# Kernel optimization log

Measured on AMD Instinct MI355X. Metric: run time of the kernel, lower is better.

## Reference

```python
import jax, jax.numpy as jnp
import numpy as np
import math

NUM_CLASSES = 80
FPN_CH = 256
STEM = [256, 256, 256, 256]
C_IN = {"c3": 64, "c4": 160, "c5": 400}


def _conv(x, w, b, pad):
    # x: (B, Cin, H, W), w: (Cout, Cin, kh, kw)
    y = jax.lax.conv_general_dilated(
        x, w, window_strides=(1, 1), padding=[(pad, pad), (pad, pad)],
        dimension_numbers=("NCHW", "OIHW", "NCHW"))
    return y + b[None, :, None, None]


def _upsample2x(x):
    # F.interpolate(scale_factor=2), default mode='nearest'
    return jnp.repeat(jnp.repeat(x, 2, axis=2), 2, axis=3)


def _flatten_hw(x):
    # (B, C, H, W) -> (B, H*W, C)
    B, C, H, W = x.shape
    return x.reshape(B, C, H * W).transpose(0, 2, 1)


def setup_inputs() -> dict:
    key = jax.random.key(0)
    ks = iter(jax.random.split(key, 64))
    d = {}
    d["c3"] = jax.random.normal(next(ks), (2, 64, 64, 64), jnp.float32)
    d["c4"] = jax.random.normal(next(ks), (2, 160, 32, 32), jnp.float32)
    d["c5"] = jax.random.normal(next(ks), (2, 400, 16, 16), jnp.float32)

    def w(shape, std):
        return jax.random.normal(next(ks), shape, jnp.float32) * std

    # FPN lateral 1x1 convs and output 3x3 convs (default torch init ~ small)
    for lvl, cin in C_IN.items():
        n = lvl[1]
        d[f"lat{n}_w"] = w((FPN_CH, cin, 1, 1), 1.0 / math.sqrt(cin))
        d[f"lat{n}_b"] = jnp.zeros((FPN_CH,), jnp.float32)
        d[f"out{n}_w"] = w((FPN_CH, FPN_CH, 3, 3), 1.0 / math.sqrt(9 * FPN_CH))
        d[f"out{n}_b"] = jnp.zeros((FPN_CH,), jnp.float32)

    # Stem convs: init N(0, 0.01), bias 0 (per module code). Stacked (L, Cout, Cin, 3, 3).
    L = len(STEM)
    d["stem_cls_w"] = w((L, FPN_CH, FPN_CH, 3, 3), 0.01)
    d["stem_cls_b"] = jnp.zeros((L, FPN_CH), jnp.float32)
    d["stem_box_w"] = w((L, FPN_CH, FPN_CH, 3, 3), 0.01)
    d["stem_box_b"] = jnp.zeros((L, FPN_CH), jnp.float32)

    d["cls_w"] = w((NUM_CLASSES, FPN_CH, 3, 3), 1.0 / math.sqrt(9 * FPN_CH))
    d["cls_b"] = jnp.full((NUM_CLASSES,), -math.log(99.0), jnp.float32)
    d["box_w"] = w((4, FPN_CH, 3, 3), 1.0 / math.sqrt(9 * FPN_CH))
    d["box_b"] = jnp.zeros((4,), jnp.float32)
    d["ctr_w"] = w((1, FPN_CH, 3, 3), 1.0 / math.sqrt(9 * FPN_CH))
    d["ctr_b"] = jnp.zeros((1,), jnp.float32)
    return d


def reference(c3, c4, c5,
              lat3_w, lat3_b, lat4_w, lat4_b, lat5_w, lat5_b,
              out3_w, out3_b, out4_w, out4_b, out5_w, out5_b,
              stem_cls_w, stem_cls_b, stem_box_w, stem_box_b,
              cls_w, cls_b, box_w, box_b, ctr_w, ctr_b):
    # ---- FPN ----
    l3 = _conv(c3, lat3_w, lat3_b, 0)
    l4 = _conv(c4, lat4_w, lat4_b, 0)
    l5 = _conv(c5, lat5_w, lat5_b, 0)
    p5 = _conv(l5, out5_w, out5_b, 1)
    l4 = l4 + _upsample2x(l5)
    p4 = _conv(l4, out4_w, out4_b, 1)
    l3 = l3 + _upsample2x(l4)
    p3 = _conv(l3, out3_w, out3_b, 1)

    # ---- Prediction heads ----
    def head(feat):
        hc, hb = feat, feat
        for i in range(stem_cls_w.shape[0]):
            hc = jax.nn.relu(_conv(hc, stem_cls_w[i], stem_cls_b[i], 1))
            hb = jax.nn.relu(_conv(hb, stem_box_w[i], stem_box_b[i], 1))
        cls = _flatten_hw(_conv(hc, cls_w, cls_b, 1))      # (B, HW, num_classes)
        box = _flatten_hw(_conv(hb, box_w, box_b, 1))      # (B, HW, 4)
        ctr = _flatten_hw(_conv(hb, ctr_w, ctr_b, 1))      # (B, HW, 1)
        return cls, box, ctr

    outs = [head(p) for p in (p3, p4, p5)]
    cls_all = jnp.concatenate([o[0] for o in outs], axis=1)
    box_all = jnp.concatenate([o[1] for o in outs], axis=1)
    ctr_all = jnp.concatenate([o[2] for o in outs], axis=1)
    # pack: (B, total_locations, num_classes + 4 + 1)
    return jnp.concatenate([cls_all, box_all, ctr_all], axis=-1)
```

## Files before the change

### kernel.cpp

```cpp
#include <hip/hip_runtime.h>

typedef unsigned short u16;
typedef __attribute__((ext_vector_type(8))) __bf16 bf16x8;
typedef __attribute__((ext_vector_type(16))) float f32x16;

__device__ __forceinline__ float bf2f(u16 u) {
  union { unsigned i; float f; } x; x.i = ((unsigned)u) << 16; return x.f;
}
__device__ __forceinline__ u16 f2bf(float f) {
  union { float f; unsigned i; } x; x.f = f;
  unsigned r = x.i + 0x7FFFu + ((x.i >> 16) & 1u);
  return (u16)(r >> 16);
}
__device__ __forceinline__ bf16x8 ld8(const u16* p) {
  union { int2 i2[2]; bf16x8 v; } u;
  u.i2[0] = *(const int2*)p;
  u.i2[1] = *(const int2*)(p + 4);
  return u.v;
}

struct WJob { const float* src; u16* dst; int Cin, Cout, taps, NC, Cpad, special; };
struct WArgs {
  WJob j[16];
  const float *box_w, *ctr_w;
  const float *cls_b, *box_b, *ctr_b;
  float *bcls, *bbc;
};

__global__ __launch_bounds__(256) void wtrans_kernel(WArgs a) {
  WJob jb = a.j[blockIdx.y];
  int count = jb.taps * jb.NC * jb.Cpad * 64;
  for (int e = blockIdx.x * 256 + threadIdx.x; e < count; e += gridDim.x * 256) {
    int cw = e & 63;
    int r = e >> 6;
    int n = r % jb.Cpad;
    int q = r / jb.Cpad;
    int t = q % jb.taps;
    int cc = q / jb.taps;
    int ci = cc * 64 + cw;
    int nl = (n & ~63) + 2 * (n & 31) + ((n >> 5) & 1);
    float v = 0.f;
    if (jb.special) {
      if (ci < jb.Cin) {
        if (nl < 4) v = a.box_w[((size_t)nl * jb.Cin + ci) * jb.taps + t];
        else if (nl == 4) v = a.ctr_w[(size_t)ci * jb.taps + t];
      }
    } else if (nl < jb.Cout && ci < jb.Cin) {
      v = jb.src[((size_t)nl * jb.Cin + ci) * jb.taps + t];
    }
    jb.dst[e] = f2bf(v);
  }
  if (blockIdx.y == 0 && blockIdx.x == 0) {
    int t = threadIdx.x;
    if (t < 128) a.bcls[t] = (t < 80) ? a.cls_b[t] : 0.f;
    else if (t < 192) {
      int n = t - 128;
      a.bbc[n] = (n < 4) ? a.box_b[n] : (n == 4 ? a.ctr_b[0] : 0.f);
    }
  }
}

__global__ __launch_bounds__(256) void transpose_kernel(const float* __restrict__ c3,
                                                        const float* __restrict__ c4,
                                                        const float* __restrict__ c5,
                                                        u16* __restrict__ c3t,
                                                        u16* __restrict__ c4t,
                                                        u16* __restrict__ c5t) {
  int gid = blockIdx.x * 256 + threadIdx.x;
  const float* in; u16* out; int C, HW;
  if (gid < 524288) { in = c3; out = c3t; C = 64; HW = 4096; }
  else if (gid < 851968) { gid -= 524288; in = c4; out = c4t; C = 160; HW = 1024; }
  else { gid -= 851968; if (gid >= 204800) return; in = c5; out = c5t; C = 400; HW = 256; }
  int CHW = C * HW;
  int b = gid / CHW;
  int rem = gid - b * CHW;
  int c = rem / HW;
  int pos = rem - c * HW;
  out[((size_t)b * HW + pos) * C + c] = f2bf(in[gid]);
}

__global__ __launch_bounds__(256) void upadd2_kernel(u16* __restrict__ l3, u16* __restrict__ l4n,
                                                     const u16* __restrict__ l4,
                                                     const u16* __restrict__ l5) {
  int gid = blockIdx.x * 256 + threadIdx.x;
  if (gid < 524288) {
    int c = gid & 255; int m = gid >> 8;
    int b = m >> 10, pos = m & 1023;
    int y = pos >> 5, x = pos & 31;
    int sp = (b << 8) + ((y >> 1) << 4) + (x >> 1);
    l4n[gid] = f2bf(bf2f(l4[gid]) + bf2f(l5[(size_t)sp * 256 + c]));
  } else {
    int g2 = gid - 524288;
    int c = g2 & 255; int m = g2 >> 8;
    int b = m >> 12, pos = m & 4095;
    int y = pos >> 6, x = pos & 63;
    int sp2 = (b << 10) + ((y >> 1) << 5) + (x >> 1);
    int sp4 = (b << 8) + ((y >> 2) << 4) + (x >> 2);
    l3[g2] = f2bf(bf2f(l3[g2]) + bf2f(l4[(size_t)sp2 * 256 + c]) + bf2f(l5[(size_t)sp4 * 256 + c]));
  }
}

struct ConvP {
  const u16* src[2][3];
  const u16* wT[2][3];
  const float* bias[2][3];
  void* dst[2][3];
  int H[3], W[3], lgW[3], lgHW[3], pre[3], NC[3], Crow[3], locoff[3];
  int Cpad[2], Nvalid[2], choff[2], ny[2];
  int relu, direct;
};

#define APAD 68

#define TAPX(RB) do {                                                          \
    if (kk + 1 < ktot) {                                                       \
      writeB((kk + 1) & 1, RB);                                                \
      if (kk + 3 < ktot) loadB(kk + 3, RB);                                    \
    }                                                                          \
    const u16* ar = As + hpbase * APAD + koffs;                                \
    const u16* br0 = Bs[kk & 1] + (lane & 31) * APAD + koffs;                  \
    const u16* br1 = br0 + 32 * APAD;                                          \
    _Pragma("unroll")                                                          \
    for (int ks = 0; ks < 4; ++ks) {                                           \
      bf16x8 af = ld8(ar + ks * 16);                                           \
      acc[0] = __builtin_amdgcn_mfma_f32_32x32x16_bf16(af, ld8(br0 + ks * 16), acc[0], 0, 0, 0); \
      acc[1] = __builtin_amdgcn_mfma_f32_32x32x16_bf16(af, ld8(br1 + ks * 16), acc[1], 0, 0, 0); \
    }                                                                          \
    __syncthreads();                                                           \
    ++kk; ++cc;                                                                \
    if (cc < NCv) {                                                            \
      writeA(rA);                                                              \
      if (cc + 1 < NCv) loadA(cc + 1, rA);                                     \
      __syncthreads();                                                         \
    }                                                                          \
  } while (0)

__global__ __launch_bounds__(256, 3) void conv1_kernel(ConvP p) {
  constexpr int HALO_W = 8;
  constexpr int NA = 16 * 8 * 8;
  constexpr int NSLOT = 4;
  __shared__ u16 As[128 * APAD];
  __shared__ u16 Bs[2][64 * APAD];
  const int tid = threadIdx.x;
  const int br = blockIdx.z;
  if (blockIdx.y >= p.ny[br]) return;
  const int bx = blockIdx.x;
  const int lv = (bx >= p.pre[1]) + (bx >= p.pre[2]);
  const u16* __restrict__ src = p.src[br][lv];
  const u16* __restrict__ wT = p.wT[br][lv];
  const float* bias = p.bias[br][lv];
  void* dstv = p.dst[br][lv];
  const int H = p.H[lv], W = p.W[lv];
  const int lgWv = p.lgW[lv], lgHWv = p.lgHW[lv];
  const int NCv = p.NC[lv], Crow = p.Crow[lv];
  const int Cpadv = p.Cpad[br];
  const int ktot = NCv;
  const int nt = blockIdx.y * 64;
  const int wave = tid >> 6, lane = tid & 63;

  const int pidx = bx - p.pre[lv];
  const int lgppb = lgHWv - 7;
  const int lgnpx = lgWv - 3;
  const int batch = pidx >> lgppb;
  const int pp = pidx & ((1 << lgppb) - 1);
  const int py0 = (pp >> lgnpx) << 4;
  const int px0 = (pp & ((1 << lgnpx) - 1)) << 3;
  const size_t srcb = (size_t)batch * (1 << lgHWv) * Crow;

  f32x16 acc[2];
#pragma unroll
  for (int i = 0; i < 16; ++i) { acc[0][i] = 0.f; acc[1][i] = 0.f; }

  const int ml = wave * 32 + (lane & 31);
  const int my = ml >> 3, mx = ml & 7;
  const int koffs = (lane >> 5) << 3;
  const int hpbase = my * HALO_W + mx;

  int4 rA[NSLOT];
  int4 rB0[2], rB1[2];

  auto loadA = [&](int cc2, int4* r) {
    int kb = cc2 << 6;
#pragma unroll
    for (int s = 0; s < NSLOT; ++s) {
      int idx = s * 256 + tid;
      int4 v = make_int4(0, 0, 0, 0);
      int pos = idx >> 3, part = idx & 7;
      int hy = pos >> 3, hx = pos & 7;
      int gy = py0 + hy, gx = px0 + hx;
      int ch = kb + (part << 3);
      if ((unsigned)gy < (unsigned)H && (unsigned)gx < (unsigned)W && ch < Crow)
        v = *(const int4*)(src + srcb + (size_t)((gy << lgWv) + gx) * Crow + ch);
      r[s] = v;
    }
  };
  auto writeA = [&](const int4* r) {
#pragma unroll
    for (int s = 0; s < NSLOT; ++s) {
      int idx = s * 256 + tid;
      int pos = idx >> 3, part = idx & 7;
      u16* d = As + pos * APAD + (part << 3);
      *(int2*)d = make_int2(r[s].x, r[s].y);
      *(int2*)(d + 4) = make_int2(r[s].z, r[s].w);
    }
  };
  auto loadB = [&](int j, int4* r) {
    const u16* wsrc = wT + (((size_t)j * Cpadv + nt) << 6);
    r[0] = *(const int4*)(wsrc + ((tid >> 3) << 6) + ((tid & 7) << 3));
    r[1] = *(const int4*)(wsrc + (((tid >> 3) + 32) << 6) + ((tid & 7) << 3));
  };
  auto writeB = [&](int bufi, const int4* r) {
    u16* bb = Bs[bufi];
    u16* d0 = bb + (tid >> 3) * APAD + ((tid & 7) << 3);
    u16* d1 = bb + ((tid >> 3) + 32) * APAD + ((tid & 7) << 3);
    *(int2*)d0 = make_int2(r[0].x, r[0].y);
    *(int2*)(d0 + 4) = make_int2(r[0].z, r[0].w);
    *(int2*)d1 = make_int2(r[1].x, r[1].y);
    *(int2*)(d1 + 4) = make_int2(r[1].z, r[1].w);
  };

  loadA(0, rA);
  loadB(0, rB0);
  if (ktot > 1) loadB(1, rB1);
  writeA(rA);
  writeB(0, rB0);
  if (ktot > 2) loadB(2, rB0);
  if (NCv > 1) loadA(1, rA);
  __syncthreads();

  int kk = 0, cc = 0;
  while (true) {
    TAPX(rB1);
    if (kk >= ktot) break;
    TAPX(rB0);
    if (kk >= ktot) break;
  }

  const int col = lane & 31;
  const int rbs = 4 * (lane >> 5);
  const float bv0 = bias[nt + 2 * col];
  const float bv1 = bias[nt + 2 * col + 1];
#pragma unroll
  for (int r = 0; r < 16; ++r) {
    int m2 = wave * 32 + rbs + (r & 3) + 8 * (r >> 2);
    int posi = ((py0 + (m2 >> 3)) << lgWv) + px0 + (m2 & 7);
    float v0 = acc[0][r] + bv0;
    float v1 = acc[1][r] + bv1;
    unsigned pk = (unsigned)f2bf(v0) | ((unsigned)f2bf(v1) << 16);
    *(unsigned*)((u16*)dstv + ((size_t)(batch << lgHWv) + posi) * 256 + nt + 2 * col) = pk;
  }
}

#define TAP9(T, S) do {                                                        \
    constexpr int hpo_ = ((T) / 3 - 1) * 10 + ((T) % 3 - 1);                   \
    const u16* ar = As + (hpbase + hpo_) * APAD + koffs;                       \
    const u16* br0 = Bs[S] + (lane & 31) * APAD + koffs;                       \
    const u16* br1 = br0 + 32 * APAD;                                          \
    _Pragma("unroll")                                                          \
    for (int ks = 0; ks < 4; ++ks) {                                           \
      bf16x8 af = ld8(ar + ks * 16);                                           \
      acc[0] = __builtin_amdgcn_mfma_f32_32x32x16_bf16(af, ld8(br0 + ks * 16), acc[0], 0, 0, 0); \
      acc[1] = __builtin_amdgcn_mfma_f32_32x32x16_bf16(af, ld8(br1 + ks * 16), acc[1], 0, 0, 0); \
    }                                                                          \
  } while (0)

__global__ __launch_bounds__(256, 3) void conv9_kernel(ConvP p) {
  constexpr int HALO_W = 10;
  constexpr int NA = 18 * 10 * 8;
  constexpr int NSLOT = 6;
  __shared__ u16 As[180 * APAD];
  __shared__ u16 Bs[3][64 * APAD];
  const int tid = threadIdx.x;
  const int br = blockIdx.z;
  if (blockIdx.y >= p.ny[br]) return;
  const int bx = blockIdx.x;
  const int lv = (bx >= p.pre[1]) + (bx >= p.pre[2]);
  const u16* __restrict__ src = p.src[br][lv];
  const u16* __restrict__ wT = p.wT[br][lv];
  const float* bias = p.bias[br][lv];
  void* dstv = p.dst[br][lv];
  const int H = p.H[lv], W = p.W[lv];
  const int lgWv = p.lgW[lv], lgHWv = p.lgHW[lv];
  const int Crow = p.Crow[lv];
  const int Cpadv = p.Cpad[br];
  const int nt = blockIdx.y * 64;
  const int wave = tid >> 6, lane = tid & 63;

  const int pidx = bx - p.pre[lv];
  const int lgppb = lgHWv - 7;
  const int lgnpx = lgWv - 3;
  const int batch = pidx >> lgppb;
  const int pp = pidx & ((1 << lgppb) - 1);
  const int py0 = (pp >> lgnpx) << 4;
  const int px0 = (pp & ((1 << lgnpx) - 1)) << 3;
  const size_t srcb = (size_t)batch * (1 << lgHWv) * Crow;

  f32x16 acc[2];
#pragma unroll
  for (int i = 0; i < 16; ++i) { acc[0][i] = 0.f; acc[1][i] = 0.f; }

  const int ml = wave * 32 + (lane & 31);
  const int my = ml >> 3, mx = ml & 7;
  const int koffs = (lane >> 5) << 3;
  const int hpbase = (my + 1) * HALO_W + (mx + 1);

  int4 rA[NSLOT];
  int4 rB[6];

  auto loadA = [&](int cc2, int4* r) {
    int kb = cc2 << 6;
#pragma unroll
    for (int s = 0; s < NSLOT; ++s) {
      int idx = s * 256 + tid;
      int4 v = make_int4(0, 0, 0, 0);
      if (idx < NA) {
        int pos = idx >> 3, part = idx & 7;
        int hy = pos / HALO_W, hx = pos - hy * HALO_W;
        int gy = py0 + hy - 1, gx = px0 + hx - 1;
        int ch = kb + (part << 3);
        if ((unsigned)gy < (unsigned)H && (unsigned)gx < (unsigned)W && ch < Crow)
          v = *(const int4*)(src + srcb + (size_t)((gy << lgWv) + gx) * Crow + ch);
      }
      r[s] = v;
    }
  };
  auto writeA = [&](const int4* r) {
#pragma unroll
    for (int s = 0; s < NSLOT; ++s) {
      int idx = s * 256 + tid;
      if (idx < NA) {
        int pos = idx >> 3, part = idx & 7;
        u16* d = As + pos * APAD + (part << 3);
        *(int2*)d = make_int2(r[s].x, r[s].y);
        *(int2*)(d + 4) = make_int2(r[s].z, r[s].w);
      }
    }
  };
  auto loadB3 = [&](int j, int4* r) {
#pragma unroll
    for (int s = 0; s < 3; ++s) {
      const u16* wsrc = wT + (((size_t)(j + s) * Cpadv + nt) << 6);
      r[2 * s] = *(const int4*)(wsrc + ((tid >> 3) << 6) + ((tid & 7) << 3));
      r[2 * s + 1] = *(const int4*)(wsrc + (((tid >> 3) + 32) << 6) + ((tid & 7) << 3));
    }
  };
  auto writeB3 = [&](const int4* r) {
#pragma unroll
    for (int s = 0; s < 3; ++s) {
      u16* bb = Bs[s];
      u16* d0 = bb + (tid >> 3) * APAD + ((tid & 7) << 3);
      u16* d1 = bb + ((tid >> 3) + 32) * APAD + ((tid & 7) << 3);
      *(int2*)d0 = make_int2(r[2 * s].x, r[2 * s].y);
      *(int2*)(d0 + 4) = make_int2(r[2 * s].z, r[2 * s].w);
      *(int2*)d1 = make_int2(r[2 * s + 1].x, r[2 * s + 1].y);
      *(int2*)(d1 + 4) = make_int2(r[2 * s + 1].z, r[2 * s + 1].w);
    }
  };

  loadA(0, rA);
  loadB3(0, rB);
  writeA(rA);
  writeB3(rB);
  loadB3(3, rB);
  loadA(1, rA);
  __syncthreads();

  for (int cc = 0; cc < 4; ++cc) {
    TAP9(0, 0); TAP9(1, 1); TAP9(2, 2);
    __syncthreads();
    writeB3(rB);
    __syncthreads();
    loadB3(cc * 9 + 6, rB);
    TAP9(3, 0); TAP9(4, 1); TAP9(5, 2);
    __syncthreads();
    writeB3(rB);
    __syncthreads();
    if (cc * 9 + 9 < 36) loadB3(cc * 9 + 9, rB);
    TAP9(6, 0); TAP9(7, 1); TAP9(8, 2);
    __syncthreads();
    if (cc < 3) {
      writeB3(rB);
      writeA(rA);
      __syncthreads();
      loadB3(cc * 9 + 12, rB);
      if (cc < 2) loadA(cc + 2, rA);
    }
  }

  const int col = lane & 31;
  const int rbs = 4 * (lane >> 5);
  const int nbase = nt + 2 * col;
  const float bv0 = bias[nbase];
  const float bv1 = bias[nbase + 1];
#pragma unroll
  for (int r = 0; r < 16; ++r) {
    int m2 = wave * 32 + rbs + (r & 3) + 8 * (r >> 2);
    int posi = ((py0 + (m2 >> 3)) << lgWv) + px0 + (m2 & 7);
    float v0 = acc[0][r] + bv0;
    float v1 = acc[1][r] + bv1;
    if (p.relu) { v0 = fmaxf(v0, 0.f); v1 = fmaxf(v1, 0.f); }
    if (!p.direct) {
      unsigned pk = (unsigned)f2bf(v0) | ((unsigned)f2bf(v1) << 16);
      *(unsigned*)((u16*)dstv + ((size_t)(batch << lgHWv) + posi) * 256 + nbase) = pk;
    } else {
      float* dd = (float*)dstv + ((size_t)(batch * 5376 + p.locoff[lv] + posi)) * 85 + p.choff[br];
      if (nbase < p.Nvalid[br]) dd[nbase] = v0;
      if (nbase + 1 < p.Nvalid[br]) dd[nbase + 1] = v1;
    }
  }
}

extern "C" void kernel_launch(void* const* d_in, const int* in_sizes, int n_in,
                              void* d_out, int out_size, void* d_ws, size_t ws_size,
                              hipStream_t stream) {
  (void)in_sizes; (void)n_in; (void)out_size; (void)ws_size;
  const float* c3 = (const float*)d_in[0];
  const float* c4 = (const float*)d_in[1];
  const float* c5 = (const float*)d_in[2];
  const float* lat_w[3] = {(const float*)d_in[3], (const float*)d_in[7], (const float*)d_in[11]};
  const float* lat_b[3] = {(const float*)d_in[4], (const float*)d_in[8], (const float*)d_in[12]};
  const float* out_w[3] = {(const float*)d_in[5], (const float*)d_in[9], (const float*)d_in[13]};
  const float* out_b[3] = {(const float*)d_in[6], (const float*)d_in[10], (const float*)d_in[14]};
  const float* scw = (const float*)d_in[15];
  const float* scb = (const float*)d_in[16];
  const float* sbw = (const float*)d_in[17];
  const float* sbb = (const float*)d_in[18];
  const float* clsw = (const float*)d_in[19];
  const float* clsb = (const float*)d_in[20];
  const float* boxw = (const float*)d_in[21];
  const float* boxb = (const float*)d_in[22];
  const float* ctrw = (const float*)d_in[23];
  const float* ctrb = (const float*)d_in[24];
  float* out = (float*)d_out;
  u16* ws = (u16*)d_ws;

  size_t o = 0;
  auto alloc = [&](size_t n) { size_t r = o; o += (n + 127) & ~(size_t)127; return ws + r; };

  u16* c3t = alloc(524288);
  u16* c4t = alloc(327680);
  u16* c5t = alloc(204800);
  u16* l3 = alloc(2097152);
  u16* l4 = alloc(524288);
  u16* l4n = alloc(524288);
  u16* l5 = alloc(131072);
  u16* p3 = alloc(2097152);
  u16* p4 = alloc(524288);
  u16* p5 = alloc(131072);
  const size_t hsz[3] = {2097152, 524288, 131072};
  u16 *hc[2][3], *hb[2][3];
  for (int ab = 0; ab < 2; ++ab)
    for (int lvv = 0; lvv < 3; ++lvv) { hc[ab][lvv] = alloc(hsz[lvv]); hb[ab][lvv] = alloc(hsz[lvv]); }
  const int latCin[3] = {64, 160, 400};
  const int latNC[3] = {1, 3, 7};
  u16* wl[3]; for (int i = 0; i < 3; ++i) wl[i] = alloc((size_t)latNC[i] * 256 * 64);
  u16* wo[3]; for (int i = 0; i < 3; ++i) wo[i] = alloc(589824);
  u16* wsc[4]; for (int i = 0; i < 4; ++i) wsc[i] = alloc(589824);
  u16* wsb[4]; for (int i = 0; i < 4; ++i) wsb[i] = alloc(589824);
  u16* wcls = alloc(294912);
  u16* wbc = alloc(147456);
  float* bcls = (float*)alloc(256);
  float* bbc = (float*)alloc(128);
  alloc(2048);

  WArgs wa;
  int ji = 0;
  for (int i = 0; i < 3; ++i) wa.j[ji++] = WJob{lat_w[i], wl[i], latCin[i], 256, 1, latNC[i], 256, 0};
  for (int i = 0; i < 3; ++i) wa.j[ji++] = WJob{out_w[i], wo[i], 256, 256, 9, 4, 256, 0};
  for (int i = 0; i < 4; ++i) wa.j[ji++] = WJob{scw + (size_t)i * 589824, wsc[i], 256, 256, 9, 4, 256, 0};
  for (int i = 0; i < 4; ++i) wa.j[ji++] = WJob{sbw + (size_t)i * 589824, wsb[i], 256, 256, 9, 4, 256, 0};
  wa.j[ji++] = WJob{clsw, wcls, 256, 80, 9, 4, 128, 0};
  wa.j[ji++] = WJob{nullptr, wbc, 256, 5, 9, 4, 64, 1};
  wa.box_w = boxw; wa.ctr_w = ctrw;
  wa.cls_b = clsb; wa.box_b = boxb; wa.ctr_b = ctrb; wa.bcls = bcls; wa.bbc = bbc;
  wtrans_kernel<<<dim3(96, 16), dim3(256), 0, stream>>>(wa);

  transpose_kernel<<<dim3(4128), dim3(256), 0, stream>>>(c3, c4, c5, c3t, c4t, c5t);

  const int Hs[3] = {64, 32, 16};
  const int lgWs[3] = {6, 5, 4}, lgHWs[3] = {12, 10, 8};
  auto setLv = [&](ConvP& p, int i, int lvv) {
    p.H[i] = Hs[lvv]; p.W[i] = Hs[lvv]; p.lgW[i] = lgWs[lvv]; p.lgHW[i] = lgHWs[lvv];
  };

  {
    ConvP p{};
    const u16* srcs[3] = {c3t, c4t, c5t};
    u16* dsts[3] = {l3, l4, l5};
    for (int i = 0; i < 3; ++i) {
      p.src[0][i] = srcs[i]; p.wT[0][i] = wl[i]; p.bias[0][i] = lat_b[i]; p.dst[0][i] = dsts[i];
      setLv(p, i, i);
      p.NC[i] = latNC[i]; p.Crow[i] = latCin[i]; p.locoff[i] = 0;
    }
    p.pre[0] = 0; p.pre[1] = 64; p.pre[2] = 80;
    p.Cpad[0] = 256; p.Nvalid[0] = 0; p.choff[0] = 0; p.ny[0] = 4;
    p.relu = 0; p.direct = 0;
    conv1_kernel<<<dim3(84, 4, 1), dim3(256), 0, stream>>>(p);
  }

  upadd2_kernel<<<dim3(10240), dim3(256), 0, stream>>>(l3, l4n, l4, l5);

  {
    ConvP p{};
    const u16* srcs[3] = {l3, l4n, l5};
    u16* dsts[3] = {p3, p4, p5};
    for (int i = 0; i < 3; ++i) {
      p.src[0][i] = srcs[i]; p.wT[0][i] = wo[i]; p.bias[0][i] = out_b[i]; p.dst[0][i] = dsts[i];
      setLv(p, i, i);
      p.NC[i] = 4; p.Crow[i] = 256; p.locoff[i] = 0;
    }
    p.pre[0] = 0; p.pre[1] = 64; p.pre[2] = 80;
    p.Cpad[0] = 256; p.Nvalid[0] = 0; p.choff[0] = 0; p.ny[0] = 4;
    p.relu = 0; p.direct = 0;
    conv9_kernel<<<dim3(84, 4, 1), dim3(256), 0, stream>>>(p);
  }

  u16* pin[3] = {p3, p4, p5};
  for (int i = 0; i < 4; ++i) {
    ConvP p{};
    int di = i & 1;
    for (int lvv = 0; lvv < 3; ++lvv) {
      const u16 *s0, *s1;
      if (i == 0) { s0 = pin[lvv]; s1 = pin[lvv]; }
      else { int si = (i - 1) & 1; s0 = hc[si][lvv]; s1 = hb[si][lvv]; }
      p.src[0][lvv] = s0; p.src[1][lvv] = s1;
      p.wT[0][lvv] = wsc[i]; p.wT[1][lvv] = wsb[i];
      p.bias[0][lvv] = scb + i * 256; p.bias[1][lvv] = sbb + i * 256;
      p.dst[0][lvv] = hc[di][lvv]; p.dst[1][lvv] = hb[di][lvv];
      setLv(p, lvv, lvv);
      p.NC[lvv] = 4; p.Crow[lvv] = 256; p.locoff[lvv] = 0;
    }
    p.pre[0] = 0; p.pre[1] = 64; p.pre[2] = 80;
    p.Cpad[0] = 256; p.Cpad[1] = 256;
    p.Nvalid[0] = 0; p.Nvalid[1] = 0; p.choff[0] = 0; p.choff[1] = 0;
    p.ny[0] = 4; p.ny[1] = 4;
    p.relu = 1; p.direct = 0;
    conv9_kernel<<<dim3(84, 4, 2), dim3(256), 0, stream>>>(p);
  }

  {
    const int locoffs[3] = {0, 4096, 5120};
    ConvP p{};
    for (int lvv = 0; lvv < 3; ++lvv) {
      p.src[0][lvv] = hc[1][lvv]; p.wT[0][lvv] = wcls; p.bias[0][lvv] = bcls; p.dst[0][lvv] = out;
      p.src[1][lvv] = hb[1][lvv]; p.wT[1][lvv] = wbc; p.bias[1][lvv] = bbc; p.dst[1][lvv] = out;
      setLv(p, lvv, lvv);
      p.NC[lvv] = 4; p.Crow[lvv] = 256; p.locoff[lvv] = locoffs[lvv];
    }
    p.pre[0] = 0; p.pre[1] = 64; p.pre[2] = 80;
    p.Cpad[0] = 128; p.Cpad[1] = 64;
    p.Nvalid[0] = 80; p.Nvalid[1] = 5;
    p.choff[0] = 0; p.choff[1] = 80;
    p.ny[0] = 2; p.ny[1] = 1;
    p.relu = 0; p.direct = 1;
    conv9_kernel<<<dim3(84, 2, 2), dim3(256), 0, stream>>>(p);
  }
}
```

Before: 360.9 us.

## Swizzle conv9 LDS layout, vectorize upsample-add, merge weight and input prep kernels

```diff
diff --git a/kernel.cpp b/kernel.cpp
--- a/kernel.cpp
+++ b/kernel.cpp
@@ -17,6 +17,9 @@
   u.i2[0] = *(const int2*)p;
   u.i2[1] = *(const int2*)(p + 4);
   return u.v;
+}
+__device__ __forceinline__ bf16x8 as_bf(int4 v) {
+  union { int4 i; bf16x8 b; } u; u.i = v; return u.b;
 }
 
 struct WJob { const float* src; u16* dst; int Cin, Cout, taps, NC, Cpad, special; };
@@ -25,78 +28,90 @@
   const float *box_w, *ctr_w;
   const float *cls_b, *box_b, *ctr_b;
   float *bcls, *bbc;
+  const float *tc3, *tc4, *tc5;
+  u16 *tc3t, *tc4t, *tc5t;
 };
 
-__global__ __launch_bounds__(256) void wtrans_kernel(WArgs a) {
-  WJob jb = a.j[blockIdx.y];
-  int count = jb.taps * jb.NC * jb.Cpad * 64;
-  for (int e = blockIdx.x * 256 + threadIdx.x; e < count; e += gridDim.x * 256) {
-    int cw = e & 63;
-    int r = e >> 6;
-    int n = r % jb.Cpad;
-    int q = r / jb.Cpad;
-    int t = q % jb.taps;
-    int cc = q / jb.taps;
-    int ci = cc * 64 + cw;
-    int nl = (n & ~63) + 2 * (n & 31) + ((n >> 5) & 1);
-    float v = 0.f;
-    if (jb.special) {
-      if (ci < jb.Cin) {
-        if (nl < 4) v = a.box_w[((size_t)nl * jb.Cin + ci) * jb.taps + t];
-        else if (nl == 4) v = a.ctr_w[(size_t)ci * jb.taps + t];
+__global__ __launch_bounds__(256) void prep_kernel(WArgs a) {
+  if (blockIdx.y < 16) {
+    WJob jb = a.j[blockIdx.y];
+    int count = jb.taps * jb.NC * jb.Cpad * 64;
+    for (int e = blockIdx.x * 256 + threadIdx.x; e < count; e += gridDim.x * 256) {
+      int cw = e & 63;
+      int r = e >> 6;
+      int n = r % jb.Cpad;
+      int q = r / jb.Cpad;
+      int t = q % jb.taps;
+      int cc = q / jb.taps;
+      int ci = cc * 64 + cw;
+      int nl = (n & ~63) + 2 * (n & 31) + ((n >> 5) & 1);
+      float v = 0.f;
+      if (jb.special) {
+        if (ci < jb.Cin) {
+          if (nl < 4) v = a.box_w[((size_t)nl * jb.Cin + ci) * jb.taps + t];
+          else if (nl == 4) v = a.ctr_w[(size_t)ci * jb.taps + t];
+        }
+      } else if (nl < jb.Cout && ci < jb.Cin) {
+        v = jb.src[((size_t)nl * jb.Cin + ci) * jb.taps + t];
       }
-    } else if (nl < jb.Cout && ci < jb.Cin) {
-      v = jb.src[((size_t)nl * jb.Cin + ci) * jb.taps + t];
-    }
-    jb.dst[e] = f2bf(v);
-  }
-  if (blockIdx.y == 0 && blockIdx.x == 0) {
-    int t = threadIdx.x;
-    if (t < 128) a.bcls[t] = (t < 80) ? a.cls_b[t] : 0.f;
-    else if (t < 192) {
-      int n = t - 128;
-      a.bbc[n] = (n < 4) ? a.box_b[n] : (n == 4 ? a.ctr_b[0] : 0.f);
-    }
-  }
-}
-
-__global__ __launch_bounds__(256) void transpose_kernel(const float* __restrict__ c3,
-                                                        const float* __restrict__ c4,
-                                                        const float* __restrict__ c5,
-                                                        u16* __restrict__ c3t,
-                                                        u16* __restrict__ c4t,
-                                                        u16* __restrict__ c5t) {
-  int gid = blockIdx.x * 256 + threadIdx.x;
-  const float* in; u16* out; int C, HW;
-  if (gid < 524288) { in = c3; out = c3t; C = 64; HW = 4096; }
-  else if (gid < 851968) { gid -= 524288; in = c4; out = c4t; C = 160; HW = 1024; }
-  else { gid -= 851968; if (gid >= 204800) return; in = c5; out = c5t; C = 400; HW = 256; }
-  int CHW = C * HW;
-  int b = gid / CHW;
-  int rem = gid - b * CHW;
-  int c = rem / HW;
-  int pos = rem - c * HW;
-  out[((size_t)b * HW + pos) * C + c] = f2bf(in[gid]);
+      jb.dst[e] = f2bf(v);
+    }
+    if (blockIdx.y == 0 && blockIdx.x == 0) {
+      int t = threadIdx.x;
+      if (t < 128) a.bcls[t] = (t < 80) ? a.cls_b[t] : 0.f;
+      else if (t < 192) {
+        int n = t - 128;
+        a.bbc[n] = (n < 4) ? a.box_b[n] : (n == 4 ? a.ctr_b[0] : 0.f);
+      }
+    }
+  } else {
+    for (int gid = blockIdx.x * 256 + threadIdx.x; gid < 1056768; gid += gridDim.x * 256) {
+      int g = gid;
+      const float* in; u16* out; int C, HW;
+      if (g < 524288) { in = a.tc3; out = a.tc3t; C = 64; HW = 4096; }
+      else if (g < 851968) { g -= 524288; in = a.tc4; out = a.tc4t; C = 160; HW = 1024; }
+      else { g -= 851968; in = a.tc5; out = a.tc5t; C = 400; HW = 256; }
+      int CHW = C * HW;
+      int b = g / CHW;
+      int rem = g - b * CHW;
+      int c = rem / HW;
+      int pos = rem - c * HW;
+      out[((size_t)b * HW + pos) * C + c] = f2bf(in[g]);
+    }
+  }
 }
 
 __global__ __launch_bounds__(256) void upadd2_kernel(u16* __restrict__ l3, u16* __restrict__ l4n,
                                                      const u16* __restrict__ l4,
                                                      const u16* __restrict__ l5) {
   int gid = blockIdx.x * 256 + threadIdx.x;
-  if (gid < 524288) {
-    int c = gid & 255; int m = gid >> 8;
+  if (gid < 65536) {
+    int cg = (gid & 31) << 3;
+    int m = gid >> 5;
     int b = m >> 10, pos = m & 1023;
     int y = pos >> 5, x = pos & 31;
     int sp = (b << 8) + ((y >> 1) << 4) + (x >> 1);
-    l4n[gid] = f2bf(bf2f(l4[gid]) + bf2f(l5[(size_t)sp * 256 + c]));
+    union { int4 v; u16 s[8]; } A, B, O;
+    A.v = *(const int4*)(l4 + (size_t)m * 256 + cg);
+    B.v = *(const int4*)(l5 + (size_t)sp * 256 + cg);
+#pragma unroll
+    for (int i = 0; i < 8; ++i) O.s[i] = f2bf(bf2f(A.s[i]) + bf2f(B.s[i]));
+    *(int4*)(l4n + (size_t)m * 256 + cg) = O.v;
   } else {
-    int g2 = gid - 524288;
-    int c = g2 & 255; int m = g2 >> 8;
+    int g2 = gid - 65536;
+    int cg = (g2 & 31) << 3;
+    int m = g2 >> 5;
     int b = m >> 12, pos = m & 4095;
     int y = pos >> 6, x = pos & 63;
     int sp2 = (b << 10) + ((y >> 1) << 5) + (x >> 1);
     int sp4 = (b << 8) + ((y >> 2) << 4) + (x >> 2);
-    l3[g2] = f2bf(bf2f(l3[g2]) + bf2f(l4[(size_t)sp2 * 256 + c]) + bf2f(l5[(size_t)sp4 * 256 + c]));
+    union { int4 v; u16 s[8]; } A, B, C2, O;
+    A.v = *(const int4*)(l3 + (size_t)m * 256 + cg);
+    B.v = *(const int4*)(l4 + (size_t)sp2 * 256 + cg);
+    C2.v = *(const int4*)(l5 + (size_t)sp4 * 256 + cg);
+#pragma unroll
+    for (int i = 0; i < 8; ++i) O.s[i] = f2bf(bf2f(A.s[i]) + bf2f(B.s[i]) + bf2f(C2.s[i]));
+    *(int4*)(l3 + (size_t)m * 256 + cg) = O.v;
   }
 }
 
@@ -251,16 +266,21 @@
   }
 }
 
+#define APAD9 72
+
 #define TAP9(T, S) do {                                                        \
     constexpr int hpo_ = ((T) / 3 - 1) * 10 + ((T) % 3 - 1);                   \
-    const u16* ar = As + (hpbase + hpo_) * APAD + koffs;                       \
-    const u16* br0 = Bs[S] + (lane & 31) * APAD + koffs;                       \
-    const u16* br1 = br0 + 32 * APAD;                                          \
+    const int hp = hpbase + hpo_;                                              \
+    const u16* ar = As + hp * APAD9;                                           \
+    const u16* b0r = Bs[S] + brow * APAD9;                                     \
+    const u16* b1r = b0r + 32 * APAD9;                                         \
     _Pragma("unroll")                                                          \
     for (int ks = 0; ks < 4; ++ks) {                                           \
-      bf16x8 af = ld8(ar + ks * 16);                                           \
-      acc[0] = __builtin_amdgcn_mfma_f32_32x32x16_bf16(af, ld8(br0 + ks * 16), acc[0], 0, 0, 0); \
-      acc[1] = __builtin_amdgcn_mfma_f32_32x32x16_bf16(af, ld8(br1 + ks * 16), acc[1], 0, 0, 0); \
+      const int g = g0 + 2 * ks;                                               \
+      bf16x8 af = as_bf(*(const int4*)(ar + (((g + hp) & 7) << 3)));           \
+      const int bo = ((g + brow) & 7) << 3;                                    \
+      acc[0] = __builtin_amdgcn_mfma_f32_32x32x16_bf16(af, as_bf(*(const int4*)(b0r + bo)), acc[0], 0, 0, 0); \
+      acc[1] = __builtin_amdgcn_mfma_f32_32x32x16_bf16(af, as_bf(*(const int4*)(b1r + bo)), acc[1], 0, 0, 0); \
     }                                                                          \
   } while (0)
 
@@ -268,8 +288,8 @@
   constexpr int HALO_W = 10;
   constexpr int NA = 18 * 10 * 8;
   constexpr int NSLOT = 6;
-  __shared__ u16 As[180 * APAD];
-  __shared__ u16 Bs[3][64 * APAD];
+  __shared__ __align__(16) u16 As[180 * APAD9];
+  __shared__ __align__(16) u16 Bs[3][64 * APAD9];
   const int tid = threadIdx.x;
   const int br = blockIdx.z;
   if (blockIdx.y >= p.ny[br]) return;
@@ -301,7 +321,8 @@
 
   const int ml = wave * 32 + (lane & 31);
   const int my = ml >> 3, mx = ml & 7;
-  const int koffs = (lane >> 5) << 3;
+  const int g0 = lane >> 5;
+  const int brow = lane & 31;
   const int hpbase = (my + 1) * HALO_W + (mx + 1);
 
   int4 rA[NSLOT];
@@ -330,9 +351,7 @@
       int idx = s * 256 + tid;
       if (idx < NA) {
         int pos = idx >> 3, part = idx & 7;
-        u16* d = As + pos * APAD + (part << 3);
-        *(int2*)d = make_int2(r[s].x, r[s].y);
-        *(int2*)(d + 4) = make_int2(r[s].z, r[s].w);
+        *(int4*)(As + pos * APAD9 + (((part + pos) & 7) << 3)) = r[s];
       }
     }
   };
@@ -345,15 +364,13 @@
     }
   };
   auto writeB3 = [&](const int4* r) {
+    const int r0 = tid >> 3, part = tid & 7;
+    const int o0 = r0 * APAD9 + (((part + r0) & 7) << 3);
+    const int o1 = o0 + 32 * APAD9;
 #pragma unroll
     for (int s = 0; s < 3; ++s) {
-      u16* bb = Bs[s];
-      u16* d0 = bb + (tid >> 3) * APAD + ((tid & 7) << 3);
-      u16* d1 = bb + ((tid >> 3) + 32) * APAD + ((tid & 7) << 3);
-      *(int2*)d0 = make_int2(r[2 * s].x, r[2 * s].y);
-      *(int2*)(d0 + 4) = make_int2(r[2 * s].z, r[2 * s].w);
-      *(int2*)d1 = make_int2(r[2 * s + 1].x, r[2 * s + 1].y);
-      *(int2*)(d1 + 4) = make_int2(r[2 * s + 1].z, r[2 * s + 1].w);
+      *(int4*)(Bs[s] + o0) = r[2 * s];
+      *(int4*)(Bs[s] + o1) = r[2 * s + 1];
     }
   };
 
@@ -473,9 +490,9 @@
   wa.j[ji++] = WJob{nullptr, wbc, 256, 5, 9, 4, 64, 1};
   wa.box_w = boxw; wa.ctr_w = ctrw;
   wa.cls_b = clsb; wa.box_b = boxb; wa.ctr_b = ctrb; wa.bcls = bcls; wa.bbc = bbc;
-  wtrans_kernel<<<dim3(96, 16), dim3(256), 0, stream>>>(wa);
-
-  transpose_kernel<<<dim3(4128), dim3(256), 0, stream>>>(c3, c4, c5, c3t, c4t, c5t);
+  wa.tc3 = c3; wa.tc4 = c4; wa.tc5 = c5;
+  wa.tc3t = c3t; wa.tc4t = c4t; wa.tc5t = c5t;
+  prep_kernel<<<dim3(256, 17), dim3(256), 0, stream>>>(wa);
 
   const int Hs[3] = {64, 32, 16};
   const int lgWs[3] = {6, 5, 4}, lgHWs[3] = {12, 10, 8};
@@ -498,7 +515,7 @@
     conv1_kernel<<<dim3(84, 4, 1), dim3(256), 0, stream>>>(p);
   }
 
-  upadd2_kernel<<<dim3(10240), dim3(256), 0, stream>>>(l3, l4n, l4, l5);
+  upadd2_kernel<<<dim3(1280), dim3(256), 0, stream>>>(l3, l4n, l4, l5);
 
   {
     ConvP p{};
```

New measurement: 522.7 us. +44.8%, slower.
